# Kernel tuning notes

Measured on AMD Instinct MI355X. Metric: run time of the kernel, lower is better.

## Reference

```python
import jax, jax.numpy as jnp
import numpy as np

D_MODEL, D_K, D_V, H, GRID = 512, 64, 64, 8, 196
B = 4


def setup_inputs() -> dict:
    key = jax.random.key(0)
    ks = jax.random.split(key, 12)
    s = 0.02
    return {
        "queries": jax.random.normal(ks[0], (B, GRID, D_MODEL), jnp.float32),
        "keys": jax.random.normal(ks[1], (B, GRID, D_MODEL), jnp.float32),
        "values": jax.random.normal(ks[2], (B, GRID, D_MODEL), jnp.float32),
        "Wq": jax.random.normal(ks[3], (H * D_K, D_MODEL), jnp.float32) * s,
        "bq": jnp.zeros((H * D_K,), jnp.float32),
        "Wk": jax.random.normal(ks[4], (H * D_K, D_MODEL), jnp.float32) * s,
        "bk": jnp.zeros((H * D_K,), jnp.float32),
        "Wv": jax.random.normal(ks[5], (H * D_V, D_MODEL), jnp.float32) * s,
        "bv": jnp.zeros((H * D_V,), jnp.float32),
        "Wo": jax.random.normal(ks[6], (D_MODEL, H * D_V), jnp.float32) * s,
        "bo": jnp.zeros((D_MODEL,), jnp.float32),
        "scale": jnp.ones((1, H, GRID, GRID), jnp.float32) / np.sqrt(D_K).astype(np.float32),
    }


def reference(queries, keys, values, Wq, bq, Wk, bk, Wv, bv, Wo, bo, scale):
    b, nq, _ = queries.shape
    nk = values.shape[1]
    # linear projections (torch nn.Linear: x @ W.T + b)
    q_sig = queries @ Wq.T + bq          # (b, nq, h*dk)
    k_p = keys @ Wk.T + bk               # (b, nk, h*dk)
    v_p = values @ Wv.T + bv             # (b, nk, h*dv)
    # elementwise q*k interaction (b, nq, nk, h*dk)
    att_e = q_sig[:, :, None, :] * k_p[:, None, :, :]
    # sigmoid-gated values
    v_g = jax.nn.sigmoid(att_e) * v_p[:, None, :, :]
    v = v_g.reshape(b, nq, nk, H, D_K).transpose(0, 3, 1, 2, 4)      # (b,h,nq,nk,dk)
    att = att_e.reshape(b, nq, nk, H, D_K).transpose(0, 3, 1, 2, 4)  # (b,h,nq,nk,dk)
    att = att.sum(-1) * scale            # (b,h,nq,nk)
    p = jax.nn.softmax(att, axis=-1)     # dropout is identity in eval mode
    # (att.unsqueeze(-2) @ v).squeeze(-2)
    image = jnp.einsum("bhqk,bhqkd->bhqd", p, v)
    image = image.transpose(0, 2, 1, 3).reshape(b, nq, H * D_V)
    out = image @ Wo.T + bo              # (b, nq, d_model)
    out = jax.nn.sigmoid(q_sig * out) * out
    return out
```

## Files before the change

kernel.cpp:

```cpp
#include <hip/hip_runtime.h>
#include <hip/hip_bf16.h>
#include <math.h>

#define NQ 196
#define BATCH 4
#define HD 512
#define NH 8
#define DK 64
#define MROWS 784
#define MPAD 832

typedef __attribute__((ext_vector_type(8))) short short8;
typedef __attribute__((ext_vector_type(4))) short short4v;
typedef __attribute__((ext_vector_type(4))) float float4v;

__device__ __forceinline__ float b2f(short s) {
  return __uint_as_float(((unsigned)(unsigned short)s) << 16);
}
__device__ __forceinline__ short f2b(float x) {
  return __builtin_bit_cast(short, __float2bfloat16(x));
}
__device__ __forceinline__ float fexp2(float x) {
  float r; asm("v_exp_f32 %0, %1" : "=v"(r) : "v"(x)); return r;
}
__device__ __forceinline__ float frcp(float x) {
  float r; asm("v_rcp_f32 %0, %1" : "=v"(r) : "v"(x)); return r;
}
__device__ __forceinline__ void cvt4(float4 v, short4v& hi, short4v& lo) {
  float x[4] = {v.x, v.y, v.z, v.w};
  #pragma unroll
  for (int i = 0; i < 4; ++i) {
    hi[i] = f2b(x[i]);
    lo[i] = f2b(x[i] - b2f(hi[i]));
  }
}
__device__ __forceinline__ void gload_lds16(const void* g, void* l) {
  __builtin_amdgcn_global_load_lds(
      (const __attribute__((address_space(1))) unsigned int*)g,
      (__attribute__((address_space(3))) unsigned int*)l, 16, 0, 0);
}

struct WSplitArgs { const float* src[4]; short* hi[4]; short* lo[4]; };

__global__ __launch_bounds__(256)
void wsplit_kernel(WSplitArgs a) {
  const int seg = blockIdx.x >> 7;
  const size_t off = (size_t)(blockIdx.x & 127) * 2048 + (size_t)threadIdx.x * 8;
  const float* src = a.src[seg] + off;
  float4 v0 = *(const float4*)(src);
  float4 v1 = *(const float4*)(src + 4);
  short4v h0, l0, h1, l1;
  cvt4(v0, h0, l0); cvt4(v1, h1, l1);
  short8 vh = {h0[0],h0[1],h0[2],h0[3],h1[0],h1[1],h1[2],h1[3]};
  short8 vl = {l0[0],l0[1],l0[2],l0[3],l1[0],l1[1],l1[2],l1[3]};
  *(short8*)(a.hi[seg] + off) = vh;
  *(short8*)(a.lo[seg] + off) = vl;
}


struct ProjArgs {
  const float* X[3]; const short* Wh[3]; const short* Wl[3]; const float* bias[3];
  float* Cf[3]; short* Ch[3]; short* Cl[3];
};

__global__ __launch_bounds__(512)
void proj_gemm(ProjArgs p, int M, int N, int K) {
  const int z = blockIdx.z;
  const float* __restrict__ X  = p.X[z];
  const short* __restrict__ Wh = p.Wh[z];
  const short* __restrict__ Wl = p.Wl[z];

  __shared__ short smem[24576];
  short* const A_ = smem;
  short* const B_ = smem + 8192;
  float* const redC = (float*)smem;

  const int t = threadIdx.x;
  const int g = t >> 8;
  const int tt = t & 255;
  const int ln = t & 63, lm = ln & 15, quad = ln >> 4;
  const int w = (t >> 6) & 3;
  const int m0 = blockIdx.x * 32, n0 = blockIdx.y * 64;
  const int kb = g << 8;

  const int aRow = tt >> 3, aK = (tt & 7) << 2;
  const int ar = min(m0 + aRow, M - 1);
  const float* Ap = X + (size_t)ar * K + kb + aK;
  const int aIdx = aRow * 32 + aK;
  const int bRow = tt >> 2, bK = (tt & 3) << 3;
  const short* Bph = Wh + (size_t)(n0 + bRow) * K + kb + bK;
  const short* Bpl = Wl + (size_t)(n0 + bRow) * K + kb + bK;

  const int wm = (w & 1) << 4, wn = (w >> 1) << 5;
  float4v acc[2] = {{0.f,0.f,0.f,0.f},{0.f,0.f,0.f,0.f}};

  const int T = 8;
  float4 ra = *(const float4*)Ap;
  gload_lds16(Bph, &B_[((g << 1) + 0) * 4096 + 0 * 2048 + tt * 8]);
  gload_lds16(Bpl, &B_[((g << 1) + 0) * 4096 + 1 * 2048 + tt * 8]);
  {
    short4v ahi, alo; cvt4(ra, ahi, alo);
    *(short4v*)&A_[((g << 1) + 0) * 2048 + 0 * 1024 + aIdx] = ahi;
    *(short4v*)&A_[((g << 1) + 0) * 2048 + 1 * 1024 + aIdx] = alo;
  }

  for (int kt = 0; kt < T; ++kt) {
    const int buf = kt & 1;
    __syncthreads();
    if (kt + 1 < T) {
      ra = *(const float4*)(Ap + (size_t)(kt + 1) * 32);
      const int nb = buf ^ 1;
      gload_lds16(Bph + (size_t)(kt + 1) * 32, &B_[((g << 1) + nb) * 4096 + 0 * 2048 + tt * 8]);
      gload_lds16(Bpl + (size_t)(kt + 1) * 32, &B_[((g << 1) + nb) * 4096 + 1 * 2048 + tt * 8]);
    }
    const short* Ab = &A_[((g << 1) + buf) * 2048];
    const short* Bb = &B_[((g << 1) + buf) * 4096];
    short8 fah = *(const short8*)&Ab[0 * 1024 + (wm + lm) * 32 + (quad << 3)];
    short8 fal = *(const short8*)&Ab[1 * 1024 + (wm + lm) * 32 + (quad << 3)];
    #pragma unroll
    for (int ni = 0; ni < 2; ++ni) {
      short8 fbh = *(const short8*)&Bb[0 * 2048 + (wn + (ni << 4) + lm) * 32 + (quad << 3)];
      short8 fbl = *(const short8*)&Bb[1 * 2048 + (wn + (ni << 4) + lm) * 32 + (quad << 3)];
      acc[ni] = __builtin_amdgcn_mfma_f32_16x16x32_bf16(fah, fbh, acc[ni], 0,0,0);
      acc[ni] = __builtin_amdgcn_mfma_f32_16x16x32_bf16(fah, fbl, acc[ni], 0,0,0);
      acc[ni] = __builtin_amdgcn_mfma_f32_16x16x32_bf16(fal, fbh, acc[ni], 0,0,0);
    }
    if (kt + 1 < T) {
      const int nb = buf ^ 1;
      short4v ahi, alo; cvt4(ra, ahi, alo);
      *(short4v*)&A_[((g << 1) + nb) * 2048 + 0 * 1024 + aIdx] = ahi;
      *(short4v*)&A_[((g << 1) + nb) * 2048 + 1 * 1024 + aIdx] = alo;
    }
  }

  __syncthreads();
  if (g == 1) {
    #pragma unroll
    for (int ni = 0; ni < 2; ++ni)
      *(float4v*)&redC[tt * 8 + ni * 4] = acc[ni];
  }
  __syncthreads();
  if (g == 0) {
    const float* bias = p.bias[z];
    float* Cf = p.Cf[z]; short* Ch = p.Ch[z]; short* Cl = p.Cl[z];
    #pragma unroll
    for (int ni = 0; ni < 2; ++ni) {
      const int n = n0 + wn + (ni << 4) + lm;
      const float bv = bias[n];
      #pragma unroll
      for (int r = 0; r < 4; ++r) {
        const int m = m0 + wm + (quad << 2) + r;
        if (m < M) {
          const float c = acc[ni][r] + redC[tt * 8 + ni * 4 + r] + bv;
          if (Cf) Cf[(size_t)m * N + n] = c;
          if (Ch) {
            const short hi = f2b(c);
            Ch[(size_t)m * N + n] = hi;
            Cl[(size_t)m * N + n] = f2b(c - b2f(hi));
          }
        }
      }
    }
  }
}

__global__ __launch_bounds__(512)
void out_gemm(const float* __restrict__ part, const short* __restrict__ Wh,
              const short* __restrict__ Wl, const float* __restrict__ bias,
              const float* __restrict__ qsg, float* __restrict__ C,
              int M, int N, int K) {
  __shared__ short smem[24576];
  short* const A_ = smem;
  short* const B_ = smem + 8192;
  float* const redC = (float*)smem;

  const int t = threadIdx.x;
  const int g = t >> 8;
  const int tt = t & 255;
  const int ln = t & 63, lm = ln & 15, quad = ln >> 4;
  const int w = (t >> 6) & 3;
  const int m0 = blockIdx.x * 32, n0 = blockIdx.y * 64;
  const int kb = g << 8;
  const size_t NELF = (size_t)MROWS * HD;

  const int aRow = tt >> 3, aK = (tt & 7) << 2;
  const int ar = min(m0 + aRow, M - 1);
  const float* Ap = part + (size_t)ar * K + kb + aK;
  const int aIdx = aRow * 32 + aK;
  const int bRow = tt >> 2, bK = (tt & 3) << 3;
  const short* Bph = Wh + (size_t)(n0 + bRow) * K + kb + bK;
  const short* Bpl = Wl + (size_t)(n0 + bRow) * K + kb + bK;

  const int wm = (w & 1) << 4, wn = (w >> 1) << 5;
  float4v acc[2] = {{0.f,0.f,0.f,0.f},{0.f,0.f,0.f,0.f}};

  const int T = 8;
  float4 s0 = *(const float4*)(Ap);
  float4 s1 = *(const float4*)(Ap + NELF);
  float4 s2 = *(const float4*)(Ap + 2 * NELF);
  float4 s3 = *(const float4*)(Ap + 3 * NELF);
  gload_lds16(Bph, &B_[((g << 1) + 0) * 4096 + 0 * 2048 + tt * 8]);
  gload_lds16(Bpl, &B_[((g << 1) + 0) * 4096 + 1 * 2048 + tt * 8]);
  {
    float4 ra = make_float4(s0.x+s1.x+s2.x+s3.x, s0.y+s1.y+s2.y+s3.y,
                            s0.z+s1.z+s2.z+s3.z, s0.w+s1.w+s2.w+s3.w);
    short4v ahi, alo; cvt4(ra, ahi, alo);
    *(short4v*)&A_[((g << 1) + 0) * 2048 + 0 * 1024 + aIdx] = ahi;
    *(short4v*)&A_[((g << 1) + 0) * 2048 + 1 * 1024 + aIdx] = alo;
  }

  for (int kt = 0; kt < T; ++kt) {
    const int buf = kt & 1;
    __syncthreads();
    if (kt + 1 < T) {
      const size_t ko = (size_t)(kt + 1) * 32;
      s0 = *(const float4*)(Ap + ko);
      s1 = *(const float4*)(Ap + NELF + ko);
      s2 = *(const float4*)(Ap + 2 * NELF + ko);
      s3 = *(const float4*)(Ap + 3 * NELF + ko);
      const int nb = buf ^ 1;
      gload_lds16(Bph + ko, &B_[((g << 1) + nb) * 4096 + 0 * 2048 + tt * 8]);
      gload_lds16(Bpl + ko, &B_[((g << 1) + nb) * 4096 + 1 * 2048 + tt * 8]);
    }
    const short* Ab = &A_[((g << 1) + buf) * 2048];
    const short* Bb = &B_[((g << 1) + buf) * 4096];
    short8 fah = *(const short8*)&Ab[0 * 1024 + (wm + lm) * 32 + (quad << 3)];
    short8 fal = *(const short8*)&Ab[1 * 1024 + (wm + lm) * 32 + (quad << 3)];
    #pragma unroll
    for (int ni = 0; ni < 2; ++ni) {
      short8 fbh = *(const short8*)&Bb[0 * 2048 + (wn + (ni << 4) + lm) * 32 + (quad << 3)];
      short8 fbl = *(const short8*)&Bb[1 * 2048 + (wn + (ni << 4) + lm) * 32 + (quad << 3)];
      acc[ni] = __builtin_amdgcn_mfma_f32_16x16x32_bf16(fah, fbh, acc[ni], 0,0,0);
      acc[ni] = __builtin_amdgcn_mfma_f32_16x16x32_bf16(fah, fbl, acc[ni], 0,0,0);
      acc[ni] = __builtin_amdgcn_mfma_f32_16x16x32_bf16(fal, fbh, acc[ni], 0,0,0);
    }
    if (kt + 1 < T) {
      const int nb = buf ^ 1;
      float4 ra = make_float4(s0.x+s1.x+s2.x+s3.x, s0.y+s1.y+s2.y+s3.y,
                              s0.z+s1.z+s2.z+s3.z, s0.w+s1.w+s2.w+s3.w);
      short4v ahi, alo; cvt4(ra, ahi, alo);
      *(short4v*)&A_[((g << 1) + nb) * 2048 + 0 * 1024 + aIdx] = ahi;
      *(short4v*)&A_[((g << 1) + nb) * 2048 + 1 * 1024 + aIdx] = alo;
    }
  }

  __syncthreads();
  if (g == 1) {
    #pragma unroll
    for (int ni = 0; ni < 2; ++ni)
      *(float4v*)&redC[tt * 8 + ni * 4] = acc[ni];
  }
  __syncthreads();
  if (g == 0) {
    #pragma unroll
    for (int ni = 0; ni < 2; ++ni) {
      const int n = n0 + wn + (ni << 4) + lm;
      const float bv = bias[n];
      #pragma unroll
      for (int r = 0; r < 4; ++r) {
        const int m = m0 + wm + (quad << 2) + r;
        if (m < M) {
          float c = acc[ni][r] + redC[tt * 8 + ni * 4 + r] + bv;
          const float qg = qsg[(size_t)m * N + n];
          c = __fdividef(c, 1.f + __expf(-qg * c));
          C[(size_t)m * N + n] = c;
        }
      }
    }
  }
}

__global__ __launch_bounds__(256)
void scores_softmax(const short* __restrict__ qsh, const short* __restrict__ qsl,
                    const short* __restrict__ ksh, const short* __restrict__ ksl,
                    const float* __restrict__ scg, float* __restrict__ pbuf) {
  const int q0 = blockIdx.x * 16;
  const int bh = blockIdx.y;
  const int b = bh >> 3, h = bh & 7;
  const int w = threadIdx.x >> 6, ln = threadIdx.x & 63;
  const int lm = ln & 15, quad = ln >> 4;
  const float L2E = 1.4426950408889634f;

  __shared__ float S[16][210];

  const size_t abase = ((size_t)(b * NQ) + q0 + lm) * HD + h * DK + (quad << 3);
  short8 ah0 = *(const short8*)(qsh + abase);
  short8 ah1 = *(const short8*)(qsh + abase + 32);
  short8 al0 = *(const short8*)(qsl + abase);
  short8 al1 = *(const short8*)(qsl + abase + 32);

  for (int nt = w; nt < 13; nt += 4) {
    const size_t bbase = ((size_t)(b * NQ) + nt * 16 + lm) * HD + h * DK + (quad << 3);
    short8 bh0 = *(const short8*)(ksh + bbase);
    short8 bh1 = *(const short8*)(ksh + bbase + 32);
    short8 bl0 = *(const short8*)(ksl + bbase);
    short8 bl1 = *(const short8*)(ksl + bbase + 32);
    float4v acc = {0.f, 0.f, 0.f, 0.f};
    acc = __builtin_amdgcn_mfma_f32_16x16x32_bf16(ah0, bh0, acc, 0,0,0);
    acc = __builtin_amdgcn_mfma_f32_16x16x32_bf16(ah1, bh1, acc, 0,0,0);
    acc = __builtin_amdgcn_mfma_f32_16x16x32_bf16(ah0, bl0, acc, 0,0,0);
    acc = __builtin_amdgcn_mfma_f32_16x16x32_bf16(ah1, bl1, acc, 0,0,0);
    acc = __builtin_amdgcn_mfma_f32_16x16x32_bf16(al0, bh0, acc, 0,0,0);
    acc = __builtin_amdgcn_mfma_f32_16x16x32_bf16(al1, bh1, acc, 0,0,0);
    #pragma unroll
    for (int r = 0; r < 4; ++r)
      S[(quad << 2) + r][nt * 16 + lm] = acc[r];
  }
  __syncthreads();

  for (int i = 0; i < 4; ++i) {
    const int rr = (w << 2) + i;
    const int q = q0 + rr;
    const bool qok = q < NQ;
    const float* srow = scg + ((size_t)h * NQ + (qok ? q : 0)) * NQ;
    float att[4];
    #pragma unroll
    for (int j = 0; j < 4; ++j) {
      const int c = ln + (j << 6);
      att[j] = -1e30f;
      if (c < NQ) att[j] = S[rr][c] * srow[c] * L2E;
    }
    float m = fmaxf(fmaxf(att[0], att[1]), fmaxf(att[2], att[3]));
    #pragma unroll
    for (int off = 32; off; off >>= 1) m = fmaxf(m, __shfl_xor(m, off, 64));
    float e[4], s = 0.f;
    #pragma unroll
    for (int j = 0; j < 4; ++j) { e[j] = fexp2(att[j] - m); s += e[j]; }
    #pragma unroll
    for (int off = 32; off; off >>= 1) s += __shfl_xor(s, off, 64);
    const float rinv = __fdividef(1.f, s);
    if (qok) {
      float* prow = pbuf + (((size_t)(b * NH + h) * NQ) + q) * NQ;
      #pragma unroll
      for (int j = 0; j < 4; ++j) {
        const int c = ln + (j << 6);
        if (c < NQ) prow[c] = e[j] * rinv;
      }
    }
  }
}

__global__ __launch_bounds__(256)
void pv_kernel(const float* __restrict__ qsg, const float* __restrict__ kpg,
               const float* __restrict__ vpg, const float* __restrict__ pbuf,
               float* __restrict__ part) {
  const int b  = blockIdx.y;
  const int x  = blockIdx.x;
  const int qg = x >> 3;
  const int ks = (x >> 1) & 3;
  const int dh = x & 1;
  const int q0 = qg << 2;
  const int hd = (dh << 8) + threadIdx.x;
  const int h  = hd >> 6;
  const float LOG2E = 1.4426950408889634f;

  const size_t r0 = ((size_t)(b * NQ) + q0) * HD + hd;
  float nqs[4];
  #pragma unroll
  for (int qi = 0; qi < 4; ++qi)
    nqs[qi] = -qsg[r0 + (size_t)qi * HD] * LOG2E;

  const float* kp = kpg + (size_t)b * NQ * HD + hd;
  const float* vp = vpg + (size_t)b * NQ * HD + hd;
  const float* pr = pbuf + ((size_t)(b * NH + h) * NQ + q0) * NQ;

  float acc[4] = {0.f, 0.f, 0.f, 0.f};
  const int kbeg = ks * 49;
  for (int k = kbeg; k < kbeg + 49; ++k) {
    const float kv = kp[(size_t)k * HD];
    const float vv = vp[(size_t)k * HD];
    #pragma unroll
    for (int qi = 0; qi < 4; ++qi) {
      const float e = fexp2(nqs[qi] * kv);
      const float g = vv * frcp(1.f + e);
      acc[qi] += pr[(size_t)qi * NQ + k] * g;
    }
  }
  float* dst = part + (size_t)ks * ((size_t)MROWS * HD) + r0;
  #pragma unroll
  for (int qi = 0; qi < 4; ++qi) dst[(size_t)qi * HD] = acc[qi];
}

extern "C" void kernel_launch(void* const* d_in, const int* in_sizes, int n_in,
                              void* d_out, int out_size, void* d_ws, size_t ws_size,
                              hipStream_t stream) {
  const float* queries = (const float*)d_in[0];
  const float* keys    = (const float*)d_in[1];
  const float* values  = (const float*)d_in[2];
  const float* Wq = (const float*)d_in[3];
  const float* bq = (const float*)d_in[4];
  const float* Wk = (const float*)d_in[5];
  const float* bk = (const float*)d_in[6];
  const float* Wv = (const float*)d_in[7];
  const float* bv = (const float*)d_in[8];
  const float* Wo = (const float*)d_in[9];
  const float* bo = (const float*)d_in[10];
  const float* scale = (const float*)d_in[11];

  char* base = (char*)d_ws;
  const size_t FB = sizeof(float);
  const size_t NELF  = (size_t)MROWS * HD;
  const size_t NELPS = (size_t)MPAD * HD;
  const size_t WEL   = (size_t)HD * HD;

  size_t o = 0;
  float* q_sig = (float*)(base + o); o += NELF * FB;
  float* k_p   = (float*)(base + o); o += NELF * FB;
  float* v_p   = (float*)(base + o); o += NELF * FB;
  float* pbuf  = (float*)(base + o); o += (size_t)BATCH * NH * NQ * NQ * FB;
  short* qsh = (short*)(base + o); o += NELPS * 2;
  short* qsl = (short*)(base + o); o += NELPS * 2;
  short* ksh = (short*)(base + o); o += NELPS * 2;
  short* ksl = (short*)(base + o); o += NELPS * 2;
  short* Wqh = (short*)(base + o); o += WEL * 2;
  short* Wql = (short*)(base + o); o += WEL * 2;
  short* Wkh = (short*)(base + o); o += WEL * 2;
  short* Wkl = (short*)(base + o); o += WEL * 2;
  short* Wvh = (short*)(base + o); o += WEL * 2;
  short* Wvl = (short*)(base + o); o += WEL * 2;
  short* Woh = (short*)(base + o); o += WEL * 2;
  short* Wol = (short*)(base + o); o += WEL * 2;
  float* part = (float*)(base + o); o += 4 * NELF * FB;

  WSplitArgs wa;
  wa.src[0] = Wq; wa.hi[0] = Wqh; wa.lo[0] = Wql;
  wa.src[1] = Wk; wa.hi[1] = Wkh; wa.lo[1] = Wkl;
  wa.src[2] = Wv; wa.hi[2] = Wvh; wa.lo[2] = Wvl;
  wa.src[3] = Wo; wa.hi[3] = Woh; wa.lo[3] = Wol;
  wsplit_kernel<<<512, 256, 0, stream>>>(wa);

  ProjArgs gp;
  gp.X[0] = queries; gp.Wh[0] = Wqh; gp.Wl[0] = Wql; gp.bias[0] = bq;
  gp.Cf[0] = q_sig;  gp.Ch[0] = qsh; gp.Cl[0] = qsl;
  gp.X[1] = keys;    gp.Wh[1] = Wkh; gp.Wl[1] = Wkl; gp.bias[1] = bk;
  gp.Cf[1] = k_p;    gp.Ch[1] = ksh; gp.Cl[1] = ksl;
  gp.X[2] = values;  gp.Wh[2] = Wvh; gp.Wl[2] = Wvl; gp.bias[2] = bv;
  gp.Cf[2] = v_p;    gp.Ch[2] = nullptr; gp.Cl[2] = nullptr;
  proj_gemm<<<dim3(25, HD/64, 3), 512, 0, stream>>>(gp, MROWS, HD, HD);

  scores_softmax<<<dim3(13, NH*BATCH), 256, 0, stream>>>(qsh, qsl, ksh, ksl, scale, pbuf);

  pv_kernel<<<dim3(392, BATCH), 256, 0, stream>>>(q_sig, k_p, v_p, pbuf, part);

  out_gemm<<<dim3(25, HD/64), 512, 0, stream>>>(part, Woh, Wol, bo, q_sig,
                                                (float*)d_out, MROWS, HD, HD);
}
```

Baseline: 145.2 us.

## Fuse softmax scores with gated PV reduction and reuse projection GEMM for output

Merges the scores/softmax kernel and the PV kernel into one attention kernel. Probabilities stay in shared memory and the four key-split partials are reduced in LDS, so the full attention-probability buffer and the 4-way partial sum buffer in global memory are no longer needed. The output projection now reuses the generic projection GEMM with an optional sigmoid-gate epilogue and reads a single image buffer. The cost is fewer blocks for the gated PV stage (13x8x4 instead of 392x4) and 16 accumulators per thread, which may reduce parallelism and occupancy.

```diff
diff --git a/kernel.cpp b/kernel.cpp
--- a/kernel.cpp
+++ b/kernel.cpp
@@ -57,14 +57,13 @@
   *(short8*)(a.lo[seg] + off) = vl;
 }
 
-
-struct ProjArgs {
+struct GemmArgs {
   const float* X[3]; const short* Wh[3]; const short* Wl[3]; const float* bias[3];
-  float* Cf[3]; short* Ch[3]; short* Cl[3];
+  float* Cf[3]; short* Ch[3]; short* Cl[3]; const float* gate[3];
 };
 
 __global__ __launch_bounds__(512)
-void proj_gemm(ProjArgs p, int M, int N, int K) {
+void mgemm(GemmArgs p, int M, int N, int K) {
   const int z = blockIdx.z;
   const float* __restrict__ X  = p.X[z];
   const short* __restrict__ Wh = p.Wh[z];
@@ -142,6 +141,7 @@
   __syncthreads();
   if (g == 0) {
     const float* bias = p.bias[z];
+    const float* gate = p.gate[z];
     float* Cf = p.Cf[z]; short* Ch = p.Ch[z]; short* Cl = p.Cl[z];
     #pragma unroll
     for (int ni = 0; ni < 2; ++ni) {
@@ -151,7 +151,11 @@
       for (int r = 0; r < 4; ++r) {
         const int m = m0 + wm + (quad << 2) + r;
         if (m < M) {
-          const float c = acc[ni][r] + redC[tt * 8 + ni * 4 + r] + bv;
+          float c = acc[ni][r] + redC[tt * 8 + ni * 4 + r] + bv;
+          if (gate) {
+            const float qg = gate[(size_t)m * N + n];
+            c = __fdividef(c, 1.f + __expf(-qg * c));
+          }
           if (Cf) Cf[(size_t)m * N + n] = c;
           if (Ch) {
             const short hi = f2b(c);
@@ -164,124 +168,22 @@
   }
 }
 
-__global__ __launch_bounds__(512)
-void out_gemm(const float* __restrict__ part, const short* __restrict__ Wh,
-              const short* __restrict__ Wl, const float* __restrict__ bias,
-              const float* __restrict__ qsg, float* __restrict__ C,
-              int M, int N, int K) {
-  __shared__ short smem[24576];
-  short* const A_ = smem;
-  short* const B_ = smem + 8192;
-  float* const redC = (float*)smem;
-
-  const int t = threadIdx.x;
-  const int g = t >> 8;
-  const int tt = t & 255;
-  const int ln = t & 63, lm = ln & 15, quad = ln >> 4;
-  const int w = (t >> 6) & 3;
-  const int m0 = blockIdx.x * 32, n0 = blockIdx.y * 64;
-  const int kb = g << 8;
-  const size_t NELF = (size_t)MROWS * HD;
-
-  const int aRow = tt >> 3, aK = (tt & 7) << 2;
-  const int ar = min(m0 + aRow, M - 1);
-  const float* Ap = part + (size_t)ar * K + kb + aK;
-  const int aIdx = aRow * 32 + aK;
-  const int bRow = tt >> 2, bK = (tt & 3) << 3;
-  const short* Bph = Wh + (size_t)(n0 + bRow) * K + kb + bK;
-  const short* Bpl = Wl + (size_t)(n0 + bRow) * K + kb + bK;
-
-  const int wm = (w & 1) << 4, wn = (w >> 1) << 5;
-  float4v acc[2] = {{0.f,0.f,0.f,0.f},{0.f,0.f,0.f,0.f}};
-
-  const int T = 8;
-  float4 s0 = *(const float4*)(Ap);
-  float4 s1 = *(const float4*)(Ap + NELF);
-  float4 s2 = *(const float4*)(Ap + 2 * NELF);
-  float4 s3 = *(const float4*)(Ap + 3 * NELF);
-  gload_lds16(Bph, &B_[((g << 1) + 0) * 4096 + 0 * 2048 + tt * 8]);
-  gload_lds16(Bpl, &B_[((g << 1) + 0) * 4096 + 1 * 2048 + tt * 8]);
-  {
-    float4 ra = make_float4(s0.x+s1.x+s2.x+s3.x, s0.y+s1.y+s2.y+s3.y,
-                            s0.z+s1.z+s2.z+s3.z, s0.w+s1.w+s2.w+s3.w);
-    short4v ahi, alo; cvt4(ra, ahi, alo);
-    *(short4v*)&A_[((g << 1) + 0) * 2048 + 0 * 1024 + aIdx] = ahi;
-    *(short4v*)&A_[((g << 1) + 0) * 2048 + 1 * 1024 + aIdx] = alo;
-  }
-
-  for (int kt = 0; kt < T; ++kt) {
-    const int buf = kt & 1;
-    __syncthreads();
-    if (kt + 1 < T) {
-      const size_t ko = (size_t)(kt + 1) * 32;
-      s0 = *(const float4*)(Ap + ko);
-      s1 = *(const float4*)(Ap + NELF + ko);
-      s2 = *(const float4*)(Ap + 2 * NELF + ko);
-      s3 = *(const float4*)(Ap + 3 * NELF + ko);
-      const int nb = buf ^ 1;
-      gload_lds16(Bph + ko, &B_[((g << 1) + nb) * 4096 + 0 * 2048 + tt * 8]);
-      gload_lds16(Bpl + ko, &B_[((g << 1) + nb) * 4096 + 1 * 2048 + tt * 8]);
-    }
-    const short* Ab = &A_[((g << 1) + buf) * 2048];
-    const short* Bb = &B_[((g << 1) + buf) * 4096];
-    short8 fah = *(const short8*)&Ab[0 * 1024 + (wm + lm) * 32 + (quad << 3)];
-    short8 fal = *(const short8*)&Ab[1 * 1024 + (wm + lm) * 32 + (quad << 3)];
-    #pragma unroll
-    for (int ni = 0; ni < 2; ++ni) {
-      short8 fbh = *(const short8*)&Bb[0 * 2048 + (wn + (ni << 4) + lm) * 32 + (quad << 3)];
-      short8 fbl = *(const short8*)&Bb[1 * 2048 + (wn + (ni << 4) + lm) * 32 + (quad << 3)];
-      acc[ni] = __builtin_amdgcn_mfma_f32_16x16x32_bf16(fah, fbh, acc[ni], 0,0,0);
-      acc[ni] = __builtin_amdgcn_mfma_f32_16x16x32_bf16(fah, fbl, acc[ni], 0,0,0);
-      acc[ni] = __builtin_amdgcn_mfma_f32_16x16x32_bf16(fal, fbh, acc[ni], 0,0,0);
-    }
-    if (kt + 1 < T) {
-      const int nb = buf ^ 1;
-      float4 ra = make_float4(s0.x+s1.x+s2.x+s3.x, s0.y+s1.y+s2.y+s3.y,
-                              s0.z+s1.z+s2.z+s3.z, s0.w+s1.w+s2.w+s3.w);
-      short4v ahi, alo; cvt4(ra, ahi, alo);
-      *(short4v*)&A_[((g << 1) + nb) * 2048 + 0 * 1024 + aIdx] = ahi;
-      *(short4v*)&A_[((g << 1) + nb) * 2048 + 1 * 1024 + aIdx] = alo;
-    }
-  }
-
-  __syncthreads();
-  if (g == 1) {
-    #pragma unroll
-    for (int ni = 0; ni < 2; ++ni)
-      *(float4v*)&redC[tt * 8 + ni * 4] = acc[ni];
-  }
-  __syncthreads();
-  if (g == 0) {
-    #pragma unroll
-    for (int ni = 0; ni < 2; ++ni) {
-      const int n = n0 + wn + (ni << 4) + lm;
-      const float bv = bias[n];
-      #pragma unroll
-      for (int r = 0; r < 4; ++r) {
-        const int m = m0 + wm + (quad << 2) + r;
-        if (m < M) {
-          float c = acc[ni][r] + redC[tt * 8 + ni * 4 + r] + bv;
-          const float qg = qsg[(size_t)m * N + n];
-          c = __fdividef(c, 1.f + __expf(-qg * c));
-          C[(size_t)m * N + n] = c;
-        }
-      }
-    }
-  }
-}
-
 __global__ __launch_bounds__(256)
-void scores_softmax(const short* __restrict__ qsh, const short* __restrict__ qsl,
-                    const short* __restrict__ ksh, const short* __restrict__ ksl,
-                    const float* __restrict__ scg, float* __restrict__ pbuf) {
+void attn_fused(const short* __restrict__ qsh, const short* __restrict__ qsl,
+                const short* __restrict__ ksh, const short* __restrict__ ksl,
+                const float* __restrict__ qsg, const float* __restrict__ kpg,
+                const float* __restrict__ vpg, const float* __restrict__ scg,
+                float* __restrict__ img) {
   const int q0 = blockIdx.x * 16;
-  const int bh = blockIdx.y;
-  const int b = bh >> 3, h = bh & 7;
-  const int w = threadIdx.x >> 6, ln = threadIdx.x & 63;
+  const int h  = blockIdx.y;
+  const int b  = blockIdx.z;
+  const int t  = threadIdx.x;
+  const int w = t >> 6, ln = t & 63;
   const int lm = ln & 15, quad = ln >> 4;
   const float L2E = 1.4426950408889634f;
 
   __shared__ float S[16][210];
+  __shared__ float R[4][16][64];
 
   const size_t abase = ((size_t)(b * NQ) + q0 + lm) * HD + h * DK + (quad << 3);
   short8 ah0 = *(const short8*)(qsh + abase);
@@ -329,56 +231,55 @@
     #pragma unroll
     for (int off = 32; off; off >>= 1) s += __shfl_xor(s, off, 64);
     const float rinv = __fdividef(1.f, s);
-    if (qok) {
-      float* prow = pbuf + (((size_t)(b * NH + h) * NQ) + q) * NQ;
-      #pragma unroll
-      for (int j = 0; j < 4; ++j) {
-        const int c = ln + (j << 6);
-        if (c < NQ) prow[c] = e[j] * rinv;
-      }
-    }
-  }
-}
-
-__global__ __launch_bounds__(256)
-void pv_kernel(const float* __restrict__ qsg, const float* __restrict__ kpg,
-               const float* __restrict__ vpg, const float* __restrict__ pbuf,
-               float* __restrict__ part) {
-  const int b  = blockIdx.y;
-  const int x  = blockIdx.x;
-  const int qg = x >> 3;
-  const int ks = (x >> 1) & 3;
-  const int dh = x & 1;
-  const int q0 = qg << 2;
-  const int hd = (dh << 8) + threadIdx.x;
-  const int h  = hd >> 6;
+    #pragma unroll
+    for (int j = 0; j < 4; ++j) {
+      const int c = ln + (j << 6);
+      if (c < NQ) S[rr][c] = e[j] * rinv;
+    }
+  }
+  __syncthreads();
+
+  const int d = ln;
+  const int kg = w;
   const float LOG2E = 1.4426950408889634f;
 
-  const size_t r0 = ((size_t)(b * NQ) + q0) * HD + hd;
-  float nqs[4];
-  #pragma unroll
-  for (int qi = 0; qi < 4; ++qi)
-    nqs[qi] = -qsg[r0 + (size_t)qi * HD] * LOG2E;
-
-  const float* kp = kpg + (size_t)b * NQ * HD + hd;
-  const float* vp = vpg + (size_t)b * NQ * HD + hd;
-  const float* pr = pbuf + ((size_t)(b * NH + h) * NQ + q0) * NQ;
-
-  float acc[4] = {0.f, 0.f, 0.f, 0.f};
-  const int kbeg = ks * 49;
-  for (int k = kbeg; k < kbeg + 49; ++k) {
+  float nqs[16];
+  #pragma unroll
+  for (int qi = 0; qi < 16; ++qi) {
+    const int row = min(b * NQ + q0 + qi, MROWS - 1);
+    nqs[qi] = -qsg[(size_t)row * HD + h * DK + d] * LOG2E;
+  }
+  const float* kp = kpg + ((size_t)(b * NQ)) * HD + h * DK + d;
+  const float* vp = vpg + ((size_t)(b * NQ)) * HD + h * DK + d;
+
+  float acc[16];
+  #pragma unroll
+  for (int qi = 0; qi < 16; ++qi) acc[qi] = 0.f;
+
+  for (int k = kg * 49; k < kg * 49 + 49; ++k) {
     const float kv = kp[(size_t)k * HD];
     const float vv = vp[(size_t)k * HD];
     #pragma unroll
-    for (int qi = 0; qi < 4; ++qi) {
+    for (int qi = 0; qi < 16; ++qi) {
       const float e = fexp2(nqs[qi] * kv);
       const float g = vv * frcp(1.f + e);
-      acc[qi] += pr[(size_t)qi * NQ + k] * g;
-    }
-  }
-  float* dst = part + (size_t)ks * ((size_t)MROWS * HD) + r0;
-  #pragma unroll
-  for (int qi = 0; qi < 4; ++qi) dst[(size_t)qi * HD] = acc[qi];
+      acc[qi] += S[qi][k] * g;
+    }
+  }
+  #pragma unroll
+  for (int qi = 0; qi < 16; ++qi) R[kg][qi][d] = acc[qi];
+  __syncthreads();
+
+  #pragma unroll
+  for (int j = 0; j < 4; ++j) {
+    const int idx = t + (j << 8);
+    const int qi = idx >> 6, dd = idx & 63;
+    const int q = q0 + qi;
+    if (q < NQ) {
+      const float s = R[0][qi][dd] + R[1][qi][dd] + R[2][qi][dd] + R[3][qi][dd];
+      img[((size_t)(b * NQ) + q) * HD + h * DK + dd] = s;
+    }
+  }
 }
 
 extern "C" void kernel_launch(void* const* d_in, const int* in_sizes, int n_in,
@@ -407,7 +308,7 @@
   float* q_sig = (float*)(base + o); o += NELF * FB;
   float* k_p   = (float*)(base + o); o += NELF * FB;
   float* v_p   = (float*)(base + o); o += NELF * FB;
-  float* pbuf  = (float*)(base + o); o += (size_t)BATCH * NH * NQ * NQ * FB;
+  float* image = (float*)(base + o); o += NELF * FB;
   short* qsh = (short*)(base + o); o += NELPS * 2;
   short* qsl = (short*)(base + o); o += NELPS * 2;
   short* ksh = (short*)(base + o); o += NELPS * 2;
@@ -420,7 +321,6 @@
   short* Wvl = (short*)(base + o); o += WEL * 2;
   short* Woh = (short*)(base + o); o += WEL * 2;
   short* Wol = (short*)(base + o); o += WEL * 2;
-  float* part = (float*)(base + o); o += 4 * NELF * FB;
 
   WSplitArgs wa;
   wa.src[0] = Wq; wa.hi[0] = Wqh; wa.lo[0] = Wql;
@@ -429,19 +329,24 @@
   wa.src[3] = Wo; wa.hi[3] = Woh; wa.lo[3] = Wol;
   wsplit_kernel<<<512, 256, 0, stream>>>(wa);
 
-  ProjArgs gp;
+  GemmArgs gp;
   gp.X[0] = queries; gp.Wh[0] = Wqh; gp.Wl[0] = Wql; gp.bias[0] = bq;
-  gp.Cf[0] = q_sig;  gp.Ch[0] = qsh; gp.Cl[0] = qsl;
+  gp.Cf[0] = q_sig;  gp.Ch[0] = qsh; gp.Cl[0] = qsl; gp.gate[0] = nullptr;
   gp.X[1] = keys;    gp.Wh[1] = Wkh; gp.Wl[1] = Wkl; gp.bias[1] = bk;
-  gp.Cf[1] = k_p;    gp.Ch[1] = ksh; gp.Cl[1] = ksl;
+  gp.Cf[1] = k_p;    gp.Ch[1] = ksh; gp.Cl[1] = ksl; gp.gate[1] = nullptr;
   gp.X[2] = values;  gp.Wh[2] = Wvh; gp.Wl[2] = Wvl; gp.bias[2] = bv;
-  gp.Cf[2] = v_p;    gp.Ch[2] = nullptr; gp.Cl[2] = nullptr;
-  proj_gemm<<<dim3(25, HD/64, 3), 512, 0, stream>>>(gp, MROWS, HD, HD);
-
-  scores_softmax<<<dim3(13, NH*BATCH), 256, 0, stream>>>(qsh, qsl, ksh, ksl, scale, pbuf);
-
-  pv_kernel<<<dim3(392, BATCH), 256, 0, stream>>>(q_sig, k_p, v_p, pbuf, part);
-
-  out_gemm<<<dim3(25, HD/64), 512, 0, stream>>>(part, Woh, Wol, bo, q_sig,
-                                                (float*)d_out, MROWS, HD, HD);
-}
+  gp.Cf[2] = v_p;    gp.Ch[2] = nullptr; gp.Cl[2] = nullptr; gp.gate[2] = nullptr;
+  mgemm<<<dim3(25, HD/64, 3), 512, 0, stream>>>(gp, MROWS, HD, HD);
+
+  attn_fused<<<dim3(13, NH, BATCH), 256, 0, stream>>>(
+      qsh, qsl, ksh, ksl, q_sig, k_p, v_p, scale, image);
+
+  GemmArgs go;
+  go.X[0] = image; go.Wh[0] = Woh; go.Wl[0] = Wol; go.bias[0] = bo;
+  go.Cf[0] = (float*)d_out; go.Ch[0] = nullptr; go.Cl[0] = nullptr; go.gate[0] = q_sig;
+  for (int i = 1; i < 3; ++i) {
+    go.X[i] = nullptr; go.Wh[i] = nullptr; go.Wl[i] = nullptr; go.bias[i] = nullptr;
+    go.Cf[i] = nullptr; go.Ch[i] = nullptr; go.Cl[i] = nullptr; go.gate[i] = nullptr;
+  }
+  mgemm<<<dim3(25, HD/64, 1), 512, 0, stream>>>(go, MROWS, HD, HD);
+}
```

After: 143.1 us. About the same (-1.4%).
